# Optimization experiments

Hardware: AMD Instinct MI355X
Metric: run time of the kernel (lower is better)

## Reference

```python
import jax, jax.numpy as jnp
import numpy as np

B, T, C = 2, 2048, 1024
N_HEAD, N_KV_HEAD, N_GLOBAL_HEAD = 16, 8, 8
HEAD_DIM = C // N_HEAD  # 64
Q_PER_KV = N_HEAD // N_KV_HEAD  # 2
N_GLOBAL_KV = N_GLOBAL_HEAD // Q_PER_KV  # 4
VE_GATE_CH = 32


def setup_inputs() -> dict:
    key = jax.random.key(0)
    ks = jax.random.split(key, 8)
    x = jax.random.normal(ks[0], (B, T, C), jnp.float32)
    ve = jax.random.normal(ks[1], (B, T, N_KV_HEAD * HEAD_DIM), jnp.float32)
    # rotary cos/sin: [T, 1, head_dim//2]
    half = HEAD_DIM // 2
    inv_freq = 1.0 / (10000.0 ** (np.arange(half, dtype=np.float32) / half))
    ang = np.arange(T, dtype=np.float32)[:, None] * inv_freq[None, :]
    cos = jnp.asarray(np.cos(ang))[:, None, :]
    sin = jnp.asarray(np.sin(ang))[:, None, :]
    s = 0.02
    Wq = jax.random.normal(ks[2], (C, N_HEAD * HEAD_DIM), jnp.float32) * s
    Wk = jax.random.normal(ks[3], (C, N_KV_HEAD * HEAD_DIM), jnp.float32) * s
    Wv = jax.random.normal(ks[4], (C, N_KV_HEAD * HEAD_DIM), jnp.float32) * s
    Wproj = jax.random.normal(ks[5], (C, C), jnp.float32) * s
    Wgate = jax.random.normal(ks[6], (VE_GATE_CH, N_KV_HEAD), jnp.float32) * s
    return {"x": x, "ve": ve, "cos": cos, "sin": sin, "Wq": Wq, "Wk": Wk,
            "Wv": Wv, "Wproj": Wproj, "Wgate": Wgate, "window": 512}


def _rope(x, cos, sin):
    # x: [B,T,H,D]; cos/sin: [T,1,D/2]
    d = x.shape[-1] // 2
    x1, x2 = x[..., :d], x[..., d:]
    return jnp.concatenate([x1 * cos + x2 * sin, -x1 * sin + x2 * cos], axis=-1)


def _rmsnorm(x):
    eps = jnp.finfo(x.dtype).eps
    return x * jax.lax.rsqrt(jnp.mean(x * x, axis=-1, keepdims=True) + eps)


def _attn(q, k, v, mask):
    # q,k,v: [B,T,H,D]; mask: [T,T] bool (True = allowed)
    scale = 1.0 / jnp.sqrt(jnp.asarray(q.shape[-1], q.dtype))
    scores = jnp.einsum('bqhd,bkhd->bhqk', q, k) * scale
    scores = jnp.where(mask[None, None], scores, jnp.finfo(scores.dtype).min)
    p = jax.nn.softmax(scores, axis=-1)
    return jnp.einsum('bhqk,bkhd->bqhd', p, v)


def reference(x, ve, cos, sin, Wq, Wk, Wv, Wproj, Wgate, window):
    q = (x @ Wq).reshape(B, T, N_HEAD, HEAD_DIM)
    k = (x @ Wk).reshape(B, T, N_KV_HEAD, HEAD_DIM)
    v = (x @ Wv).reshape(B, T, N_KV_HEAD, HEAD_DIM)
    # value-embedding gate
    gate = 2.0 * jax.nn.sigmoid(x[..., :VE_GATE_CH] @ Wgate)  # [B,T,n_kv]
    v = v + gate[..., None] * ve.reshape(B, T, N_KV_HEAD, HEAD_DIM)
    q, k = _rope(q, cos, sin), _rope(k, cos, sin)
    q, k = _rmsnorm(q), _rmsnorm(k)
    # split global / local heads
    qg, ql = q[:, :, :N_GLOBAL_HEAD], q[:, :, N_GLOBAL_HEAD:]
    kg, kl = k[:, :, :N_GLOBAL_KV], k[:, :, N_GLOBAL_KV:]
    vg, vl = v[:, :, :N_GLOBAL_KV], v[:, :, N_GLOBAL_KV:]
    # GQA: expand kv heads
    kg, vg = jnp.repeat(kg, Q_PER_KV, axis=2), jnp.repeat(vg, Q_PER_KV, axis=2)
    kl, vl = jnp.repeat(kl, Q_PER_KV, axis=2), jnp.repeat(vl, Q_PER_KV, axis=2)
    i = jnp.arange(T)[:, None]
    j = jnp.arange(T)[None, :]
    causal = j <= i
    local_mask = causal & (j >= i - window)  # flash window_size=(window, 0)
    yg = _attn(qg, kg, vg, causal)
    yl = _attn(ql, kl, vl, local_mask)
    y = jnp.concatenate([yg, yl], axis=2).reshape(B, T, C)
    return y @ Wproj
```

## Files before the change

### kernel.cpp

```cpp
#include <hip/hip_runtime.h>
#include <hip/hip_bf16.h>

#define BB 2
#define TT 2048
#define CC 1024
#define NH 16
#define NKV 8
#define HD 64

typedef __attribute__((ext_vector_type(8))) short short8;
typedef __attribute__((ext_vector_type(4))) float float4v;
typedef __attribute__((ext_vector_type(4))) unsigned int uint4v;

__device__ __forceinline__ ushort f2bf(float f) {
    __hip_bfloat16 h = __float2bfloat16(f);
    union { __hip_bfloat16 h; ushort u; } v; v.h = h; return v.u;
}
__device__ __forceinline__ float bf2f(ushort u) {
    union { unsigned int i; float f; } v; v.i = ((unsigned int)u) << 16; return v.f;
}

__device__ __forceinline__ float fexp2(float x) {
#if __has_builtin(__builtin_amdgcn_exp2f)
    return __builtin_amdgcn_exp2f(x);
#else
    return __expf(x * 0.69314718056f);
#endif
}

__device__ __forceinline__ void gload16(const ushort* g, ushort* l) {
    __builtin_amdgcn_global_load_lds(
        (const __attribute__((address_space(1))) unsigned int*)g,
        (__attribute__((address_space(3))) unsigned int*)l, 16, 0, 0);
}

__device__ __forceinline__ void transpose_tile(
    const float* __restrict__ src, ushort* __restrict__ dst,
    int Kd, int Nd, int kt, int nt, float* tile )
{
    const int tid = threadIdx.x;
    {
        int r = tid >> 2, c = (tid & 3) * 16;
        #pragma unroll
        for (int i = 0; i < 4; i++) {
            float4 v = *(const float4*)&src[(size_t)(kt + r) * Nd + nt + c + i * 4];
            tile[r * 65 + c + i * 4 + 0] = v.x;
            tile[r * 65 + c + i * 4 + 1] = v.y;
            tile[r * 65 + c + i * 4 + 2] = v.z;
            tile[r * 65 + c + i * 4 + 3] = v.w;
        }
    }
    __syncthreads();
    {
        int n = tid >> 2, k = (tid & 3) * 16;
        #pragma unroll
        for (int i = 0; i < 2; i++) {
            ushort u[8];
            #pragma unroll
            for (int j = 0; j < 8; j++) u[j] = f2bf(tile[(k + i * 8 + j) * 65 + n]);
            *(uint4*)&dst[(size_t)(nt + n) * Kd + kt + k + i * 8] = *(uint4*)u;
        }
    }
}

__global__ __launch_bounds__(256) void prep_kernel(
    const float* __restrict__ x, ushort* __restrict__ xb,
    const float* __restrict__ Wq, const float* __restrict__ Wk,
    const float* __restrict__ Wv, const float* __restrict__ Wproj,
    ushort* __restrict__ WqkvT, ushort* __restrict__ WpT)
{
    __shared__ float tile[64 * 65];
    const int bid = blockIdx.x;
    if (bid < 4096) {
        int i = (bid * 256 + threadIdx.x) * 4;
        float4 v = *(const float4*)&x[i];
        xb[i + 0] = f2bf(v.x);
        xb[i + 1] = f2bf(v.y);
        xb[i + 2] = f2bf(v.z);
        xb[i + 3] = f2bf(v.w);
        return;
    }
    int t = bid - 4096;
    if (t < 256) {
        transpose_tile(Wq, WqkvT, 1024, 1024, (t >> 4) * 64, (t & 15) * 64, tile);
    } else if (t < 384) {
        t -= 256;
        transpose_tile(Wk, WqkvT + (size_t)1024 * 1024, 1024, 512, (t >> 3) * 64, (t & 7) * 64, tile);
    } else if (t < 512) {
        t -= 384;
        transpose_tile(Wv, WqkvT + (size_t)1536 * 1024, 1024, 512, (t >> 3) * 64, (t & 7) * 64, tile);
    } else {
        t -= 512;
        transpose_tile(Wproj, WpT, 1024, 1024, (t >> 4) * 64, (t & 15) * 64, tile);
    }
}

template<int BM, int OBF16>
__global__ __launch_bounds__(256) void gemm_bt_kernel(
    const ushort* __restrict__ A, const ushort* __restrict__ Bt,
    void* __restrict__ Cp, int M, int N, int K, int ldc)
{
    constexpr int RT = BM / 32;
    __shared__ ushort As[BM][32];
    __shared__ ushort Bs[128][32];

    const int m0 = blockIdx.x * BM;
    const int n0 = blockIdx.y * 128;
    const int tid = threadIdx.x;
    const int lane = tid & 63;
    const int w = tid >> 6;
    const int lr = lane & 15, lc = lane >> 4;
    const int wm = (w >> 1) * (BM / 2), wn = (w & 1) * 64;

    float4v acc[RT][4] = {};

    for (int k0 = 0; k0 < K; k0 += 32) {
        #pragma unroll
        for (int s = 0; s < BM / 64; s++) {
            int rb = w * (BM / 4) + s * 16;
            gload16(&A[(size_t)(m0 + rb + (lane >> 2)) * K + k0 + (lane & 3) * 8], &As[rb][0]);
        }
        #pragma unroll
        for (int s = 0; s < 2; s++) {
            int rb = w * 32 + s * 16;
            gload16(&Bt[(size_t)(n0 + rb + (lane >> 2)) * K + k0 + (lane & 3) * 8], &Bs[rb][0]);
        }
        __syncthreads();

        short8 af[RT], bf[4];
        #pragma unroll
        for (int t = 0; t < RT; t++)
            af[t] = *(const short8*)&As[wm + t * 16 + lr][lc * 8];
        #pragma unroll
        for (int t = 0; t < 4; t++)
            bf[t] = *(const short8*)&Bs[wn + t * 16 + lr][lc * 8];
        #pragma unroll
        for (int rt = 0; rt < RT; rt++)
            #pragma unroll
            for (int ct = 0; ct < 4; ct++)
                acc[rt][ct] = __builtin_amdgcn_mfma_f32_16x16x32_bf16(af[rt], bf[ct], acc[rt][ct], 0, 0, 0);
        __syncthreads();
    }

    #pragma unroll
    for (int rt = 0; rt < RT; rt++)
        #pragma unroll
        for (int ct = 0; ct < 4; ct++)
            #pragma unroll
            for (int r = 0; r < 4; r++) {
                int row = m0 + wm + rt * 16 + lc * 4 + r;
                int col = n0 + wn + ct * 16 + lr;
                if (OBF16) ((ushort*)Cp)[(size_t)row * ldc + col] = f2bf(acc[rt][ct][r]);
                else       ((float*)Cp)[(size_t)row * ldc + col] = acc[rt][ct][r];
            }
}

__global__ __launch_bounds__(256) void qkv_post_kernel(
    const ushort* __restrict__ qkv, const float* __restrict__ x,
    const float* __restrict__ ve, const float* __restrict__ cosb,
    const float* __restrict__ sinb, const float* __restrict__ wgate,
    ushort* __restrict__ Qb, ushort* __restrict__ Kb, ushort* __restrict__ Vn)
{
    const int bt = blockIdx.x;
    const int b = bt >> 11, t = bt & 2047;
    const int tid = threadIdx.x;
    const int lane = tid & 63;
    const int w = tid >> 6;
    __shared__ float gateS[8];

    {
        int g = tid >> 5, i = tid & 31;
        float p = x[(size_t)bt * CC + i] * wgate[i * 8 + g];
        #pragma unroll
        for (int off = 16; off; off >>= 1) p += __shfl_down(p, off, 32);
        if (i == 0) gateS[g] = 2.f / (1.f + __expf(-p));
    }
    __syncthreads();

    const float c = cosb[t * 32 + (lane & 31)];
    const float s = sinb[t * 32 + (lane & 31)];
    for (int hh = w; hh < 24; hh += 4) {
        const ushort* z = &qkv[(size_t)bt * 2048 + hh * 64];
        float v = bf2f(z[lane]);
        float other = __shfl_xor(v, 32);
        float x1 = (lane < 32) ? v : other;
        float x2 = (lane < 32) ? other : v;
        float val = (lane < 32) ? (x1 * c + x2 * s) : (-x1 * s + x2 * c);
        float ss = val * val;
        #pragma unroll
        for (int off = 32; off; off >>= 1) ss += __shfl_xor(ss, off);
        float scale = rsqrtf(ss * (1.f / 64.f) + 1.1920929e-07f);
        ushort ob = f2bf(val * scale);
        if (hh < 16) Qb[(((size_t)b * NH + hh) * TT + t) * HD + lane] = ob;
        else         Kb[(((size_t)b * NKV + (hh - 16)) * TT + t) * HD + lane] = ob;
    }

    for (int e = tid; e < NKV * HD; e += 256) {
        int kh = e >> 6, d = e & 63;
        float v = bf2f(qkv[(size_t)bt * 2048 + 1536 + e]) + gateS[kh] * ve[(size_t)bt * 512 + e];
        Vn[(((size_t)b * NKV + kh) * TT + t) * HD + d] = f2bf(v);
    }
}

__global__ __launch_bounds__(256) void v_transpose_kernel(
    const ushort* __restrict__ Vn, ushort* __restrict__ Vt)
{
    __shared__ ushort tile[64][72];
    const int t0 = blockIdx.x * 64;
    const int bh = blockIdx.y;
    const ushort* src = &Vn[(size_t)bh * TT * HD + (size_t)t0 * HD];
    ushort* dst = &Vt[(size_t)bh * HD * TT + t0];
    const int tid = threadIdx.x;
    {
        int r = tid >> 2, c = (tid & 3) * 16;
        #pragma unroll
        for (int i = 0; i < 2; i++)
            *(uint4*)&tile[r][c + i * 8] = *(const uint4*)&src[(size_t)r * HD + c + i * 8];
    }
    __syncthreads();
    {
        int d = tid >> 2, c = (tid & 3) * 16;
        #pragma unroll
        for (int i = 0; i < 2; i++) {
            ushort u[8];
            #pragma unroll
            for (int j = 0; j < 8; j++) u[j] = tile[c + i * 8 + j][d];
            *(uint4*)&dst[(size_t)d * TT + c + i * 8] = *(uint4*)u;
        }
    }
}

__global__ __launch_bounds__(256) void attn_kernel(
    const ushort* __restrict__ Qb, const ushort* __restrict__ Kb,
    const ushort* __restrict__ Vt, ushort* __restrict__ Yb,
    const int* __restrict__ winp)
{
    const int gid = blockIdx.x;
    int b, h, qw;
    if (gid < 1024) { qw = 63 - (gid >> 4); h = (gid >> 1) & 7; b = gid & 1; }
    else { int j = gid - 1024; qw = 63 - (j >> 4); h = 8 + ((j >> 1) & 7); b = j & 1; }

    const int q0 = qw * 32;
    const int kvh = h >> 1;
    const bool local = (h >= 8);
    int window = *winp;
    if (window < 0 || window > TT) window = TT;
    const int tid = threadIdx.x;
    const int w = tid >> 6;
    const int lane = tid & 63;
    const int lr = lane & 15, lc = lane >> 4;

    __shared__ float4v Ol[4][4][64];
    __shared__ float Ll[4][16];

    const ushort* qbase = &Qb[(((size_t)b * NH + h) * TT + q0) * HD];
    short8 qf[2][2];
    #pragma unroll
    for (int rt = 0; rt < 2; rt++)
        #pragma unroll
        for (int xh = 0; xh < 2; xh++)
            qf[rt][xh] = *(const short8*)&qbase[(size_t)(rt * 16 + lr) * HD + xh * 32 + lc * 8];

    float4v o[2][4] = {};
    float l_[2] = {0.f, 0.f};

    const ushort* Kbase = &Kb[((size_t)b * NKV + kvh) * TT * HD];
    const ushort* Vbase = &Vt[((size_t)b * NKV + kvh) * HD * TT];

    const int qlast = q0 + 31;
    int jstart = 0;
    if (local) { int js = q0 - window; if (js > 0) jstart = js & ~63; }
    const int j0first = jstart + w * 64;

    const float ESC = 0.1803368801f;

    short8 kf[4][2];
    if (j0first <= qlast) {
        #pragma unroll
        for (int jt = 0; jt < 4; jt++) {
            const ushort* kp = &Kbase[(size_t)(j0first + jt * 16 + lr) * HD + lc * 8];
            kf[jt][0] = *(const short8*)kp;
            kf[jt][1] = *(const short8*)(kp + 32);
        }
    }

    for (int j0 = j0first; j0 <= qlast; j0 += 256) {
        short8 vf[4][2];
        #pragma unroll
        for (int ct = 0; ct < 4; ct++) {
            const ushort* vp = &Vbase[(size_t)(ct * 16 + lr) * TT + j0 + lc * 8];
            vf[ct][0] = *(const short8*)vp;
            vf[ct][1] = *(const short8*)(vp + 32);
        }
        short8 kn[4][2];
        const bool more = (j0 + 256 <= qlast);
        if (more) {
            #pragma unroll
            for (int jt = 0; jt < 4; jt++) {
                const ushort* kp = &Kbase[(size_t)(j0 + 256 + jt * 16 + lr) * HD + lc * 8];
                kn[jt][0] = *(const short8*)kp;
                kn[jt][1] = *(const short8*)(kp + 32);
            }
        }

        float4v st[2][4];
        #pragma unroll
        for (int jt = 0; jt < 4; jt++)
            #pragma unroll
            for (int rt = 0; rt < 2; rt++) {
                float4v z = {};
                z = __builtin_amdgcn_mfma_f32_16x16x32_bf16(kf[jt][0], qf[rt][0], z, 0, 0, 0);
                z = __builtin_amdgcn_mfma_f32_16x16x32_bf16(kf[jt][1], qf[rt][1], z, 0, 0, 0);
                st[rt][jt] = z;
            }

        const bool need_c = (j0 + 63 > q0);
        const bool need_w = local && (j0 < qlast - window);

        #pragma unroll
        for (int rt = 0; rt < 2; rt++) {
            const int qrow = q0 + rt * 16 + lr;
            float p[4][4];
            if (need_c || need_w) {
                #pragma unroll
                for (int jt = 0; jt < 4; jt++)
                    #pragma unroll
                    for (int r = 0; r < 4; r++) {
                        int key = j0 + jt * 16 + lc * 4 + r;
                        bool ok = (key <= qrow) && (!local || key >= qrow - window);
                        p[jt][r] = ok ? fexp2(st[rt][jt][r] * ESC) : 0.f;
                    }
            } else {
                #pragma unroll
                for (int jt = 0; jt < 4; jt++)
                    #pragma unroll
                    for (int r = 0; r < 4; r++)
                        p[jt][r] = fexp2(st[rt][jt][r] * ESC);
            }
            float s0 = (p[0][0] + p[0][1]) + (p[0][2] + p[0][3]);
            float s1 = (p[1][0] + p[1][1]) + (p[1][2] + p[1][3]);
            float s2 = (p[2][0] + p[2][1]) + (p[2][2] + p[2][3]);
            float s3 = (p[3][0] + p[3][1]) + (p[3][2] + p[3][3]);
            l_[rt] += (s0 + s1) + (s2 + s3);

            unsigned int a0, a1, b0, b1, c0, c1, d0, d1;
            asm("v_cvt_pk_bf16_f32 %0, %1, %2" : "=v"(a0) : "v"(p[0][0]), "v"(p[0][1]));
            asm("v_cvt_pk_bf16_f32 %0, %1, %2" : "=v"(a1) : "v"(p[0][2]), "v"(p[0][3]));
            asm("v_cvt_pk_bf16_f32 %0, %1, %2" : "=v"(b0) : "v"(p[1][0]), "v"(p[1][1]));
            asm("v_cvt_pk_bf16_f32 %0, %1, %2" : "=v"(b1) : "v"(p[1][2]), "v"(p[1][3]));
            asm("v_cvt_pk_bf16_f32 %0, %1, %2" : "=v"(c0) : "v"(p[2][0]), "v"(p[2][1]));
            asm("v_cvt_pk_bf16_f32 %0, %1, %2" : "=v"(c1) : "v"(p[2][2]), "v"(p[2][3]));
            asm("v_cvt_pk_bf16_f32 %0, %1, %2" : "=v"(d0) : "v"(p[3][0]), "v"(p[3][1]));
            asm("v_cvt_pk_bf16_f32 %0, %1, %2" : "=v"(d1) : "v"(p[3][2]), "v"(p[3][3]));

            asm("v_permlane32_swap_b32 %0, %1" : "+v"(a0), "+v"(b0));
            asm("v_permlane16_swap_b32 %0, %1" : "+v"(a0), "+v"(b0));
            asm("v_permlane32_swap_b32 %0, %1" : "+v"(a1), "+v"(b1));
            asm("v_permlane16_swap_b32 %0, %1" : "+v"(a1), "+v"(b1));
            asm("v_permlane32_swap_b32 %0, %1" : "+v"(c0), "+v"(d0));
            asm("v_permlane16_swap_b32 %0, %1" : "+v"(c0), "+v"(d0));
            asm("v_permlane32_swap_b32 %0, %1" : "+v"(c1), "+v"(d1));
            asm("v_permlane16_swap_b32 %0, %1" : "+v"(c1), "+v"(d1));

            uint4v u0 = {a0, a1, b0, b1};
            uint4v u1 = {c0, c1, d0, d1};
            short8 P0 = __builtin_bit_cast(short8, u0);
            short8 P1 = __builtin_bit_cast(short8, u1);

            #pragma unroll
            for (int ct = 0; ct < 4; ct++) {
                o[rt][ct] = __builtin_amdgcn_mfma_f32_16x16x32_bf16(vf[ct][0], P0, o[rt][ct], 0, 0, 0);
                o[rt][ct] = __builtin_amdgcn_mfma_f32_16x16x32_bf16(vf[ct][1], P1, o[rt][ct], 0, 0, 0);
            }
        }

        if (more) {
            #pragma unroll
            for (int jt = 0; jt < 4; jt++) {
                kf[jt][0] = kn[jt][0];
                kf[jt][1] = kn[jt][1];
            }
        }
    }

    #pragma unroll
    for (int rt = 0; rt < 2; rt++) {
        l_[rt] += __shfl_xor(l_[rt], 16);
        l_[rt] += __shfl_xor(l_[rt], 32);
    }

    #pragma unroll
    for (int rt = 0; rt < 2; rt++) {
        #pragma unroll
        for (int ct = 0; ct < 4; ct++) Ol[w][ct][lane] = o[rt][ct];
        if (lc == 0) Ll[w][lr] = l_[rt];
        __syncthreads();

        {
            const int ct = w;
            float ltot = (Ll[0][lr] + Ll[1][lr]) + (Ll[2][lr] + Ll[3][lr]);
            float inv = 1.f / fmaxf(ltot, 1e-20f);
            float4v a0 = Ol[0][ct][lane], a1 = Ol[1][ct][lane];
            float4v a2 = Ol[2][ct][lane], a3 = Ol[3][ct][lane];
            int qrow = q0 + rt * 16 + lr;
            ushort4 u;
            u.x = f2bf(((a0[0] + a1[0]) + (a2[0] + a3[0])) * inv);
            u.y = f2bf(((a0[1] + a1[1]) + (a2[1] + a3[1])) * inv);
            u.z = f2bf(((a0[2] + a1[2]) + (a2[2] + a3[2])) * inv);
            u.w = f2bf(((a0[3] + a1[3]) + (a2[3] + a3[3])) * inv);
            *(ushort4*)&Yb[((size_t)b * TT + qrow) * CC + h * 64 + ct * 16 + lc * 4] = u;
        }
        if (rt == 0) __syncthreads();
    }
}

extern "C" void kernel_launch(void* const* d_in, const int* in_sizes, int n_in,
                              void* d_out, int out_size, void* d_ws, size_t ws_size,
                              hipStream_t stream) {
    (void)in_sizes; (void)n_in; (void)out_size; (void)ws_size;
    const float* x     = (const float*)d_in[0];
    const float* ve    = (const float*)d_in[1];
    const float* cosb  = (const float*)d_in[2];
    const float* sinb  = (const float*)d_in[3];
    const float* Wq    = (const float*)d_in[4];
    const float* Wk    = (const float*)d_in[5];
    const float* Wv    = (const float*)d_in[6];
    const float* Wproj = (const float*)d_in[7];
    const float* Wgate = (const float*)d_in[8];
    const int*   winp  = (const int*)d_in[9];
    float* out = (float*)d_out;

    char* ws = (char*)d_ws;
    ushort* qkvb  = (ushort*)ws;
    ushort* Yb    = (ushort*)ws;
    ushort* xb    = (ushort*)(ws + 33554432);
    ushort* Vnb   = (ushort*)(ws + 33554432);
    ushort* WqkvT = (ushort*)(ws + 41943040);
    ushort* WpT   = (ushort*)(ws + 46137344);
    ushort* Qb    = (ushort*)(ws + 48234496);
    ushort* Kb    = (ushort*)(ws + 56623104);
    ushort* Vtb   = (ushort*)(ws + 60817408);

    dim3 blk(256);
    prep_kernel<<<dim3(4864), blk, 0, stream>>>(x, xb, Wq, Wk, Wv, Wproj, WqkvT, WpT);
    gemm_bt_kernel<128, 1><<<dim3(32, 16), blk, 0, stream>>>(xb, WqkvT, qkvb, 4096, 2048, 1024, 2048);
    qkv_post_kernel<<<dim3(BB * TT), blk, 0, stream>>>(qkvb, x, ve, cosb, sinb, Wgate, Qb, Kb, Vnb);
    v_transpose_kernel<<<dim3(TT / 64, BB * NKV), blk, 0, stream>>>(Vnb, Vtb);
    attn_kernel<<<dim3(2048), blk, 0, stream>>>(Qb, Kb, Vtb, Yb, winp);
    gemm_bt_kernel<64, 0><<<dim3(64, 8), blk, 0, stream>>>(Yb, WpT, out, 4096, 1024, 1024, 1024);
}
```

Baseline: 222.3 us.

## Fuse RoPE, RMSNorm and value-gate epilogue into QKV GEMM

Replaces the separate QKV GEMM plus post-processing kernel with one GEMM whose epilogue applies rotary embedding, RMS normalization and the value-embedding gate. Each warp's 64-column tile maps to one head, so the RMS reduction uses lane shuffles. The gate sigmoid is moved into the prep kernel and stored in a small buffer. This removes the bf16 qkv intermediate round trip and one kernel launch, at the cost of scattered 2-byte epilogue stores and extra cos/sin/ve loads inside the GEMM.

```diff
diff --git a/kernel.cpp b/kernel.cpp
--- a/kernel.cpp
+++ b/kernel.cpp
@@ -67,7 +67,9 @@
     const float* __restrict__ x, ushort* __restrict__ xb,
     const float* __restrict__ Wq, const float* __restrict__ Wk,
     const float* __restrict__ Wv, const float* __restrict__ Wproj,
-    ushort* __restrict__ WqkvT, ushort* __restrict__ WpT)
+    const float* __restrict__ wgate,
+    ushort* __restrict__ WqkvT, ushort* __restrict__ WpT,
+    float* __restrict__ gateP)
 {
     __shared__ float tile[64 * 65];
     const int bid = blockIdx.x;
@@ -78,6 +80,13 @@
         xb[i + 1] = f2bf(v.y);
         xb[i + 2] = f2bf(v.z);
         xb[i + 3] = f2bf(v.w);
+        {
+            int g = threadIdx.x >> 5, ii = threadIdx.x & 31;
+            float p = x[(size_t)bid * CC + ii] * wgate[ii * 8 + g];
+            #pragma unroll
+            for (int off = 16; off; off >>= 1) p += __shfl_down(p, off, 32);
+            if (ii == 0) gateP[bid * 8 + g] = 2.f / (1.f + __expf(-p));
+        }
         return;
     }
     int t = bid - 4096;
@@ -155,50 +164,102 @@
             }
 }
 
-__global__ __launch_bounds__(256) void qkv_post_kernel(
-    const ushort* __restrict__ qkv, const float* __restrict__ x,
-    const float* __restrict__ ve, const float* __restrict__ cosb,
-    const float* __restrict__ sinb, const float* __restrict__ wgate,
+__global__ __launch_bounds__(256) void gemm_qkv_kernel(
+    const ushort* __restrict__ A, const ushort* __restrict__ Bt,
+    const float* __restrict__ cosb, const float* __restrict__ sinb,
+    const float* __restrict__ gateP, const float* __restrict__ ve,
     ushort* __restrict__ Qb, ushort* __restrict__ Kb, ushort* __restrict__ Vn)
 {
-    const int bt = blockIdx.x;
-    const int b = bt >> 11, t = bt & 2047;
+    constexpr int K = 1024;
+    __shared__ ushort As[128][32];
+    __shared__ ushort Bs[128][32];
+
+    const int m0 = blockIdx.x * 128;
+    const int n0 = blockIdx.y * 128;
     const int tid = threadIdx.x;
     const int lane = tid & 63;
     const int w = tid >> 6;
-    __shared__ float gateS[8];
-
-    {
-        int g = tid >> 5, i = tid & 31;
-        float p = x[(size_t)bt * CC + i] * wgate[i * 8 + g];
-        #pragma unroll
-        for (int off = 16; off; off >>= 1) p += __shfl_down(p, off, 32);
-        if (i == 0) gateS[g] = 2.f / (1.f + __expf(-p));
-    }
-    __syncthreads();
-
-    const float c = cosb[t * 32 + (lane & 31)];
-    const float s = sinb[t * 32 + (lane & 31)];
-    for (int hh = w; hh < 24; hh += 4) {
-        const ushort* z = &qkv[(size_t)bt * 2048 + hh * 64];
-        float v = bf2f(z[lane]);
-        float other = __shfl_xor(v, 32);
-        float x1 = (lane < 32) ? v : other;
-        float x2 = (lane < 32) ? other : v;
-        float val = (lane < 32) ? (x1 * c + x2 * s) : (-x1 * s + x2 * c);
-        float ss = val * val;
-        #pragma unroll
-        for (int off = 32; off; off >>= 1) ss += __shfl_xor(ss, off);
-        float scale = rsqrtf(ss * (1.f / 64.f) + 1.1920929e-07f);
-        ushort ob = f2bf(val * scale);
-        if (hh < 16) Qb[(((size_t)b * NH + hh) * TT + t) * HD + lane] = ob;
-        else         Kb[(((size_t)b * NKV + (hh - 16)) * TT + t) * HD + lane] = ob;
-    }
-
-    for (int e = tid; e < NKV * HD; e += 256) {
-        int kh = e >> 6, d = e & 63;
-        float v = bf2f(qkv[(size_t)bt * 2048 + 1536 + e]) + gateS[kh] * ve[(size_t)bt * 512 + e];
-        Vn[(((size_t)b * NKV + kh) * TT + t) * HD + d] = f2bf(v);
+    const int lr = lane & 15, lc = lane >> 4;
+    const int wm = (w >> 1) * 64, wn = (w & 1) * 64;
+
+    float4v acc[4][4] = {};
+
+    for (int k0 = 0; k0 < K; k0 += 32) {
+        #pragma unroll
+        for (int s = 0; s < 2; s++) {
+            int rb = w * 32 + s * 16;
+            gload16(&A[(size_t)(m0 + rb + (lane >> 2)) * K + k0 + (lane & 3) * 8], &As[rb][0]);
+            gload16(&Bt[(size_t)(n0 + rb + (lane >> 2)) * K + k0 + (lane & 3) * 8], &Bs[rb][0]);
+        }
+        __syncthreads();
+
+        short8 af[4], bf[4];
+        #pragma unroll
+        for (int t = 0; t < 4; t++)
+            af[t] = *(const short8*)&As[wm + t * 16 + lr][lc * 8];
+        #pragma unroll
+        for (int t = 0; t < 4; t++)
+            bf[t] = *(const short8*)&Bs[wn + t * 16 + lr][lc * 8];
+        #pragma unroll
+        for (int rt = 0; rt < 4; rt++)
+            #pragma unroll
+            for (int ct = 0; ct < 4; ct++)
+                acc[rt][ct] = __builtin_amdgcn_mfma_f32_16x16x32_bf16(af[rt], bf[ct], acc[rt][ct], 0, 0, 0);
+        __syncthreads();
+    }
+
+    const int cg = n0 + wn;
+    const int hh2 = cg >> 6;
+
+    if (hh2 < 24) {
+        #pragma unroll
+        for (int rt = 0; rt < 4; rt++) {
+            #pragma unroll
+            for (int r = 0; r < 4; r++) {
+                int row = m0 + wm + rt * 16 + lc * 4 + r;
+                int b = row >> 11, t = row & 2047;
+                float v0 = acc[rt][0][r], v1 = acc[rt][1][r];
+                float v2 = acc[rt][2][r], v3 = acc[rt][3][r];
+                const float* cp = &cosb[t * 32];
+                const float* sp = &sinb[t * 32];
+                float c0 = cp[lr], s0 = sp[lr];
+                float c1 = cp[16 + lr], s1 = sp[16 + lr];
+                float r0 = v0 * c0 + v2 * s0;
+                float r1 = v1 * c1 + v3 * s1;
+                float r2 = v2 * c0 - v0 * s0;
+                float r3 = v3 * c1 - v1 * s1;
+                float ss = (r0 * r0 + r1 * r1) + (r2 * r2 + r3 * r3);
+                ss += __shfl_xor(ss, 1);
+                ss += __shfl_xor(ss, 2);
+                ss += __shfl_xor(ss, 4);
+                ss += __shfl_xor(ss, 8);
+                float sc = rsqrtf(ss * (1.f / 64.f) + 1.1920929e-07f);
+                ushort* op = (hh2 < 16)
+                    ? &Qb[(((size_t)b * NH + hh2) * TT + t) * HD]
+                    : &Kb[(((size_t)b * NKV + (hh2 - 16)) * TT + t) * HD];
+                op[lr]      = f2bf(r0 * sc);
+                op[16 + lr] = f2bf(r1 * sc);
+                op[32 + lr] = f2bf(r2 * sc);
+                op[48 + lr] = f2bf(r3 * sc);
+            }
+        }
+    } else {
+        const int kvh = hh2 - 24;
+        #pragma unroll
+        for (int rt = 0; rt < 4; rt++) {
+            #pragma unroll
+            for (int r = 0; r < 4; r++) {
+                int row = m0 + wm + rt * 16 + lc * 4 + r;
+                int b = row >> 11, t = row & 2047;
+                float g = gateP[row * 8 + kvh];
+                const float* vp = &ve[(size_t)row * 512 + kvh * 64];
+                ushort* op = &Vn[(((size_t)b * NKV + kvh) * TT + t) * HD];
+                op[lr]      = f2bf(acc[rt][0][r] + g * vp[lr]);
+                op[16 + lr] = f2bf(acc[rt][1][r] + g * vp[16 + lr]);
+                op[32 + lr] = f2bf(acc[rt][2][r] + g * vp[32 + lr]);
+                op[48 + lr] = f2bf(acc[rt][3][r] + g * vp[48 + lr]);
+            }
+        }
     }
 }
 
@@ -431,10 +492,10 @@
     float* out = (float*)d_out;
 
     char* ws = (char*)d_ws;
-    ushort* qkvb  = (ushort*)ws;
     ushort* Yb    = (ushort*)ws;
+    float*  gateP = (float*)(ws + 8388608);
+    ushort* Vnb   = (ushort*)(ws + 12582912);
     ushort* xb    = (ushort*)(ws + 33554432);
-    ushort* Vnb   = (ushort*)(ws + 33554432);
     ushort* WqkvT = (ushort*)(ws + 41943040);
     ushort* WpT   = (ushort*)(ws + 46137344);
     ushort* Qb    = (ushort*)(ws + 48234496);
@@ -442,9 +503,8 @@
     ushort* Vtb   = (ushort*)(ws + 60817408);
 
     dim3 blk(256);
-    prep_kernel<<<dim3(4864), blk, 0, stream>>>(x, xb, Wq, Wk, Wv, Wproj, WqkvT, WpT);
-    gemm_bt_kernel<128, 1><<<dim3(32, 16), blk, 0, stream>>>(xb, WqkvT, qkvb, 4096, 2048, 1024, 2048);
-    qkv_post_kernel<<<dim3(BB * TT), blk, 0, stream>>>(qkvb, x, ve, cosb, sinb, Wgate, Qb, Kb, Vnb);
+    prep_kernel<<<dim3(4864), blk, 0, stream>>>(x, xb, Wq, Wk, Wv, Wproj, Wgate, WqkvT, WpT, gateP);
+    gemm_qkv_kernel<<<dim3(32, 16), blk, 0, stream>>>(xb, WqkvT, cosb, sinb, gateP, ve, Qb, Kb, Vnb);
     v_transpose_kernel<<<dim3(TT / 64, BB * NKV), blk, 0, stream>>>(Vnb, Vtb);
     attn_kernel<<<dim3(2048), blk, 0, stream>>>(Qb, Kb, Vtb, Yb, winp);
     gemm_bt_kernel<64, 0><<<dim3(64, 8), blk, 0, stream>>>(Yb, WpT, out, 4096, 1024, 1024, 1024);
```

Result: faster. 203.1 us (-8.6%).
